# Performance work log

Hardware: AMD Instinct MI355X
Metric: run time of the kernel (lower is better)

## Reference

```python
import jax, jax.numpy as jnp
import numpy as np

AGENT_RADIUS = 0.2
SAFETY_DIST = 0.1
_ang = np.linspace(0.0, 2.0 * np.pi, 8, endpoint=False)
OBSTACLES = np.stack([10.0 * np.cos(_ang), 10.0 * np.sin(_ang), 0.5 * np.ones(8)], axis=-1).astype(np.float32)  # (x, y, r)


def _qp_solve(p, G, h):
    """Exact solve of: min_z 0.5 z^T z + p^T z  s.t. G z <= h, z in R^2.
    Equivalent to QPFunction with Q=I. Enumerates KKT candidates over active
    sets of size 0, 1, 2 (closed form in 2D) and picks the feasible optimum.
    p: [2], G: [m,2], h: [m]."""
    m = G.shape[0]
    ii, jj = np.triu_indices(m, 1)
    # active set {} -> unconstrained minimizer
    z0 = -p[None, :]                                        # [1,2]
    # active set {i}: z = -p - lam*g_i, g_i.z = h_i
    gg = jnp.sum(G * G, axis=-1)                            # [m]
    lam1 = (-(G @ p) - h) / (gg + 1e-12)
    z1 = -p[None, :] - lam1[:, None] * G                    # [m,2]
    ok1 = lam1 >= -1e-8
    # active set {i,j}: z solves 2x2 system [g_i; g_j] z = [h_i; h_j]
    Gi, Gj = G[ii], G[jj]                                   # [P,2]
    hi, hj = h[ii], h[jj]
    det = Gi[:, 0] * Gj[:, 1] - Gi[:, 1] * Gj[:, 0]
    det_ok = jnp.abs(det) > 1e-9
    ds = jnp.where(det_ok, det, 1.0)
    zx = (hi * Gj[:, 1] - hj * Gi[:, 1]) / ds
    zy = (Gi[:, 0] * hj - Gj[:, 0] * hi) / ds
    z2 = jnp.stack([zx, zy], axis=-1)                       # [P,2]
    r = -(z2 + p[None, :])                                  # A^T lam = r
    lam_i = (Gj[:, 1] * r[:, 0] - Gj[:, 0] * r[:, 1]) / ds
    lam_j = (Gi[:, 0] * r[:, 1] - Gi[:, 1] * r[:, 0]) / ds
    ok2 = det_ok & (lam_i >= -1e-8) & (lam_j >= -1e-8)
    Z = jnp.concatenate([z0, z1, z2], axis=0)               # [K,2]
    ok = jnp.concatenate([jnp.ones((1,), bool), ok1, ok2], axis=0)
    tol = 1e-6 * (1.0 + jnp.abs(h))
    feas = jnp.all(Z @ G.T <= (h + tol)[None, :], axis=-1)  # [K]
    obj = 0.5 * jnp.sum(Z * Z, axis=-1) + Z @ p
    obj = jnp.where(ok & feas, obj, jnp.inf)
    return Z[jnp.argmin(obj)]


def _forward(x, mean, std, W1, b1, W21, b21, W31, b31, W22, b22, W32, b32):
    x0 = x * std + mean                                     # de-normalized state [B,8]
    hid = jax.nn.relu(x @ W1.T + b1)
    x31 = jax.nn.relu(hid @ W21.T + b21) @ W31.T + b31      # reference control p [B,2]
    x32 = 4.0 * jax.nn.sigmoid(jax.nn.relu(hid @ W22.T + b22) @ W32.T + b32)  # CBF penalties [B,2]
    px, py, theta, v = x0[:, 0], x0[:, 1], x0[:, 2], x0[:, 3]
    ox, oy, oth, ov = x0[:, 4], x0[:, 5], x0[:, 6], x0[:, 7]
    st, ct = jnp.sin(theta), jnp.cos(theta)
    vs, vc = v * st, v * ct
    obs = jnp.asarray(OBSTACLES, x.dtype)
    # static obstacle constraints, vectorized over the n_obs obstacles
    dx = px[:, None] - obs[None, :, 0]                      # [B,n_obs]
    dy = py[:, None] - obs[None, :, 1]
    R = AGENT_RADIUS + obs[:, 2] + SAFETY_DIST
    bar = dx * dx + dy * dy - (R * R)[None, :]
    bdot = 2.0 * dx * vc[:, None] + 2.0 * dy * vs[:, None]
    Lf2b = (2.0 * v * v)[:, None]
    u1 = -2.0 * dx * vs[:, None] + 2.0 * dy * vc[:, None]
    u2 = 2.0 * dx * ct[:, None] + 2.0 * dy * st[:, None]
    G_obs = -jnp.stack([u1, u2], axis=-1)                   # [B,n_obs,2]
    s0, s1 = x32[:, 0:1], x32[:, 1:2]
    h_obs = Lf2b + (s0 + s1) * bdot + (s0 * s1) * bar       # [B,n_obs]
    # opponent constraint
    Ro = 2.0 * AGENT_RADIUS + SAFETY_DIST
    dxo, dyo = px - ox, py - oy
    so, co = jnp.sin(oth), jnp.cos(oth)
    bar_o = dxo * dxo + dyo * dyo - Ro * Ro
    bdot_o = 2.0 * dxo * (vc - ov * co) + 2.0 * dyo * (vs - ov * so)
    Lf2b_o = 2.0 * (v * v + ov * ov + 2.0 * v * ov * jnp.cos(theta - oth))
    u1o = -2.0 * dxo * vs + 2.0 * dyo * vc
    u2o = 2.0 * dxo * ct + 2.0 * dyo * st
    G_opp = -jnp.stack([u1o, u2o], axis=-1)[:, None, :]     # [B,1,2]
    h_opp = (Lf2b_o + (x32[:, 0] + x32[:, 1]) * bdot_o + x32[:, 0] * x32[:, 1] * bar_o)[:, None]
    G = jnp.concatenate([G_obs, G_opp], axis=1)             # [B,m,2]
    h = jnp.concatenate([h_obs, h_opp], axis=1)             # [B,m]
    return jax.vmap(_qp_solve)(x31, G, h)                   # [B,2]


def setup_inputs() -> dict:
    key = jax.random.key(0)
    ks = jax.random.split(key, 6)
    B, nF, H1, H2 = 65536, 8, 256, 128

    def lin(k, o, i):
        k1, k2 = jax.random.split(k)
        W = jax.random.normal(k1, (o, i), jnp.float32) / np.float32(np.sqrt(i))
        b = jax.random.normal(k2, (o,), jnp.float32) * 0.01
        return W, b

    W1, b1 = lin(ks[0], H1, nF)
    W21, b21 = lin(ks[1], H2, H1)
    W31, b31 = lin(ks[2], 2, H2)
    W22, b22 = lin(ks[3], H2, H1)
    W32, b32 = lin(ks[4], 2, H2)
    x = jax.random.normal(ks[5], (B, nF), jnp.float32)
    return {"x": x, "mean": jnp.zeros((nF,), jnp.float32), "std": jnp.ones((nF,), jnp.float32),
            "W1": W1, "b1": b1, "W21": W21, "b21": b21, "W31": W31, "b31": b31,
            "W22": W22, "b22": b22, "W32": W32, "b32": b32, "sgn": 1}


def reference(x, mean, std, W1, b1, W21, b21, W31, b31, W22, b22, W32, b32, sgn):
    # sgn==1 / training path -> batched differentiable QP solve
    return _forward(x, mean, std, W1, b1, W21, b21, W31, b31, W22, b22, W32, b32)
```

## Files before the change

### kernel.cpp

```cpp
#include <hip/hip_runtime.h>
#include <hip/hip_bf16.h>
#include <math.h>


typedef unsigned int u32;
typedef unsigned long long u64;
typedef unsigned short u16;
typedef __attribute__((ext_vector_type(8))) short short8;
typedef __attribute__((ext_vector_type(4))) float f32x4;
typedef __attribute__((ext_vector_type(2))) float f32x2;
typedef __attribute__((ext_vector_type(4))) u32 u32x4;

union Frag { short8 v; u32 u[4]; u32x4 q; };

__device__ __forceinline__ u32 packbf(float a, float b) {
    float2 f2; f2.x = a; f2.y = b;
    __hip_bfloat162 h = __float22bfloat162_rn(f2);
    union { __hip_bfloat162 h2; u32 u; } cv; cv.h2 = h;
    return cv.u;
}

__device__ const float OBX[8] = { 10.f, 7.07106781186547524f, 6.123234e-16f, -7.07106781186547524f,
                                 -10.f, -7.07106781186547524f, -1.8369702e-15f, 7.07106781186547524f };
__device__ const float OBY[8] = { 0.f, 7.07106781186547524f, 10.f, 7.07106781186547524f,
                                  1.2246468e-15f, -7.07106781186547524f, -10.f, -7.07106781186547524f };

#define PI0_ 0x2111111100000000ULL
#define PI1_ 0x5544443333322222ULL
#define PI2_ 0x7665ULL
#define PJ0_ 0x3876543287654321ULL
#define PJ1_ 0x7687658765487654ULL
#define PJ2_ 0x8878ULL
__device__ __forceinline__ int unpack4(u64 w0, u64 w1, u64 w2, int t) {
    u64 w = (t < 16) ? w0 : (t < 32) ? w1 : w2;
    return (int)((w >> ((t & 15) * 4)) & 15);
}

__global__ __launch_bounds__(256)
void prep_kernel(const float* __restrict__ W21, const float* __restrict__ W22,
                 u32* __restrict__ ws)
{
    int idx  = blockIdx.x * 256 + threadIdx.x;
    int lane = idx & 63;
    int nt   = (idx >> 6) & 7;
    int ks   = (idx >> 9) & 7;
    int head = idx >> 12;
    const float* W = head ? W22 : W21;
    int n  = nt * 16 + (lane & 15);
    int k0 = ks * 32 + (lane >> 4) * 8;
    const float* s = W + n * 256 + k0;
    u32x4 o;
    o.x = packbf(s[0], s[1]);
    o.y = packbf(s[2], s[3]);
    o.z = packbf(s[4], s[5]);
    o.w = packbf(s[6], s[7]);
    __builtin_nontemporal_store(o, (u32x4*)ws + idx);
}

__global__ __launch_bounds__(256)
void barriernet_kernel(const float* __restrict__ x,
                       const float* __restrict__ meanp,
                       const float* __restrict__ stdp,
                       const float* __restrict__ W1,
                       const float* __restrict__ b1,
                       const float* __restrict__ b21,
                       const float* __restrict__ W31,
                       const float* __restrict__ b31,
                       const float* __restrict__ b22,
                       const float* __restrict__ W32,
                       const float* __restrict__ b32,
                       const u32* __restrict__ wsB,
                       float* __restrict__ out, int Btot)
{
    const int tid  = threadIdx.x;
    const int wave = tid >> 6;
    const int lane = tid & 63;
    const int q    = lane >> 4;
    const int m    = lane & 15;
    const int blockRow = blockIdx.x * 64;

    __shared__ u32x4 stage[2048];
    __shared__ float lds_p[64][4];

    f32x4 xa0, xb0;
    {
        int R0 = blockRow + wave * 16 + m;
        const f32x4* xv0 = (const f32x4*)(x + (R0 < Btot ? R0 : 0) * 8);
        xa0 = xv0[0]; xb0 = xv0[1];
    }

    const f32x4* W1v = (const f32x4*)W1;
    const f32x4* b1v = (const f32x4*)b1;

    Frag A[8];
    #pragma unroll
    for (int ks = 0; ks < 8; ++ks) {
        int kb = ks * 32 + q * 8;
        f32x4 bA = b1v[kb >> 2];
        f32x4 bB = b1v[(kb >> 2) + 1];
        float h0[8];
        #pragma unroll
        for (int j = 0; j < 8; ++j) {
            f32x4 wa = W1v[(kb + j) * 2];
            f32x4 wb = W1v[(kb + j) * 2 + 1];
            float a0 = (j < 4) ? bA[j] : bB[j - 4];
            a0 = fmaf(wa.x, xa0.x, a0);
            a0 = fmaf(wa.y, xa0.y, a0);
            a0 = fmaf(wa.z, xa0.z, a0);
            a0 = fmaf(wa.w, xa0.w, a0);
            a0 = fmaf(wb.x, xb0.x, a0);
            a0 = fmaf(wb.y, xb0.y, a0);
            a0 = fmaf(wb.z, xb0.z, a0);
            a0 = fmaf(wb.w, xb0.w, a0);
            h0[j] = fmaxf(a0, 0.f);
        }
        #pragma unroll
        for (int t = 0; t < 4; ++t)
            A[ks].u[t] = packbf(h0[2 * t], h0[2 * t + 1]);
    }

    const u32x4* wsB4 = (const u32x4*)wsB;

    #pragma unroll 1
    for (int head = 0; head < 2; ++head) {
        const float* b2 = head ? b22 : b21;
        const float* W3 = head ? W32 : W31;
        const float* b3 = head ? b32 : b31;

        f32x4 acc[8];
        #pragma unroll
        for (int nt = 0; nt < 8; ++nt) acc[nt] = (f32x4){0.f, 0.f, 0.f, 0.f};

        #pragma unroll
        for (int half = 0; half < 2; ++half) {
            const u32x4* src = wsB4 + head * 4096 + half * 2048;
            #pragma unroll
            for (int i = 0; i < 8; ++i) {
                int fi = (wave * 8 + i) * 64 + lane;
                stage[fi] = src[fi];
            }
            __syncthreads();
            #pragma unroll
            for (int ksl = 0; ksl < 4; ++ksl) {
                const int ks = half * 4 + ksl;
                Frag Bf[8];
                #pragma unroll
                for (int nt = 0; nt < 8; ++nt)
                    Bf[nt].q = stage[ksl * 512 + nt * 64 + lane];
                #pragma unroll
                for (int nt = 0; nt < 8; ++nt)
                    acc[nt] = __builtin_amdgcn_mfma_f32_16x16x32_bf16(A[ks].v, Bf[nt].v, acc[nt], 0, 0, 0);
            }
            __syncthreads();
        }

        float pr0[4], pr1[4];
        #pragma unroll
        for (int rg = 0; rg < 4; ++rg) { pr0[rg] = 0.f; pr1[rg] = 0.f; }
        #pragma unroll
        for (int nt = 0; nt < 8; ++nt) {
            int col = nt * 16 + m;
            float b2c = b2[col];
            float w0c = W3[col];
            float w1c = W3[128 + col];
            #pragma unroll
            for (int rg = 0; rg < 4; ++rg) {
                float rv = fmaxf(acc[nt][rg] + b2c, 0.f);
                pr0[rg] = fmaf(rv, w0c, pr0[rg]);
                pr1[rg] = fmaf(rv, w1c, pr1[rg]);
            }
        }
        #pragma unroll
        for (int rg = 0; rg < 4; ++rg) {
            float v0 = pr0[rg], v1 = pr1[rg];
            #pragma unroll
            for (int off = 1; off < 16; off <<= 1) {
                v0 += __shfl_xor(v0, off, 64);
                v1 += __shfl_xor(v1, off, 64);
            }
            pr0[rg] = v0; pr1[rg] = v1;
        }
        if (m == 0) {
            #pragma unroll
            for (int rg = 0; rg < 4; ++rg) {
                int row = wave * 16 + q * 4 + rg;
                float a0 = pr0[rg] + b3[0];
                float a1 = pr1[rg] + b3[1];
                if (head == 0) {
                    lds_p[row][0] = a0;
                    lds_p[row][1] = a1;
                } else {
                    lds_p[row][2] = 4.f / (1.f + __expf(-a0));
                    lds_p[row][3] = 4.f / (1.f + __expf(-a1));
                }
            }
        }
    }
    __syncthreads();

    f32x4 (*qC)[64]  = (f32x4(*)[64])stage;
    f32x4 (*res)[64] = (f32x4(*)[64])(stage + 576);

    const int rq   = tid & 63;
    const int part = tid >> 6;
    const int R    = blockRow + rq;
    float p0 = lds_p[rq][0];
    float p1 = lds_p[rq][1];

    if (part == 0) {
        float s0 = lds_p[rq][2];
        float s1 = lds_p[rq][3];
        float xr[8];
        const float* xp = x + (R < Btot ? R : 0) * 8;
        #pragma unroll
        for (int c = 0; c < 8; ++c) xr[c] = fmaf(xp[c], stdp[c], meanp[c]);
        float px = xr[0], py = xr[1], th = xr[2], v = xr[3];
        float ox = xr[4], oy = xr[5], oth = xr[6], ov = xr[7];
        float st = __sinf(th),  ct = __cosf(th);
        float so = __sinf(oth), co = __cosf(oth);
        float vs = v * st, vc = v * ct;
        float sps = s0 + s1, ss = s0 * s1;
        float Lf2b = 2.f * v * v;
        #pragma unroll 1
        for (int k = 0; k < 8; ++k) {
            float dx = px - OBX[k], dy = py - OBY[k];
            float bar  = dx * dx + dy * dy - 0.64f;
            float bdot = 2.f * dx * vc + 2.f * dy * vs;
            float gx = 2.f * dx * vs - 2.f * dy * vc;
            float gy = -(2.f * dx * ct + 2.f * dy * st);
            float hk = Lf2b + sps * bdot + ss * bar;
            float ht = hk + 1e-6f * (1.f + fabsf(hk));
            qC[k][rq] = (f32x4){gx, gy, hk, ht};
        }
        {
            float dxo = px - ox, dyo = py - oy;
            float bar_o  = dxo * dxo + dyo * dyo - 0.25f;
            float bdot_o = 2.f * dxo * (vc - ov * co) + 2.f * dyo * (vs - ov * so);
            float Lf2b_o = 2.f * (v * v + ov * ov + 2.f * v * ov * __cosf(th - oth));
            float gx = 2.f * dxo * vs - 2.f * dyo * vc;
            float gy = -(2.f * dxo * ct + 2.f * dyo * st);
            float hk = Lf2b_o + sps * bdot_o + ss * bar_o;
            float ht = hk + 1e-6f * (1.f + fabsf(hk));
            qC[8][rq] = (f32x4){gx, gy, hk, ht};
        }
    }
    __syncthreads();

    const f32x4 C0 = qC[0][rq], C1 = qC[1][rq], C2 = qC[2][rq];
    const f32x4 C3 = qC[3][rq], C4 = qC[4][rq], C5 = qC[5][rq];
    const f32x4 C6 = qC[6][rq], C7 = qC[7][rq], C8 = qC[8][rq];

    const int c0i = (part == 0) ? 0  : (part == 1) ? 12 : (part == 2) ? 24 : 35;
    const int c1i = (part == 0) ? 12 : (part == 1) ? 24 : (part == 2) ? 35 : 46;
    float bobj = INFINITY;
    float bzx = -p0, bzy = -p1;
    #pragma unroll 2
    for (int c = c0i; c < c1i; ++c) {
        float zx, zy;
        bool pre;
        if (c == 0) {
            zx = -p0; zy = -p1; pre = true;
        } else if (c <= 9) {
            f32x4 g = qC[c - 1][rq];
            float gg  = g.x * g.x + g.y * g.y;
            float lam = (-(g.x * p0 + g.y * p1) - g.z) / (gg + 1e-12f);
            zx = -p0 - lam * g.x;
            zy = -p1 - lam * g.y;
            pre = (lam >= -1e-8f);
        } else {
            int t = c - 10;
            int pi = unpack4(PI0_, PI1_, PI2_, t);
            int pj = unpack4(PJ0_, PJ1_, PJ2_, t);
            f32x4 gi = qC[pi][rq];
            f32x4 gj = qC[pj][rq];
            float det = gi.x * gj.y - gi.y * gj.x;
            bool dok = fabsf(det) > 1e-9f;
            float ds = dok ? det : 1.0f;
            float inv = 1.0f / ds;
            zx = (gi.z * gj.y - gj.z * gi.y) * inv;
            zy = (gi.x * gj.z - gj.x * gi.z) * inv;
            float rx = -(zx + p0), ry = -(zy + p1);
            float li = (gj.y * rx - gj.x * ry) * inv;
            float lj = (gi.x * ry - gi.y * rx) * inv;
            pre = dok && (li >= -1e-8f) && (lj >= -1e-8f);
        }
        bool ok = pre;
        ok = ok && (zx * C0.x + zy * C0.y <= C0.w);
        ok = ok && (zx * C1.x + zy * C1.y <= C1.w);
        ok = ok && (zx * C2.x + zy * C2.y <= C2.w);
        ok = ok && (zx * C3.x + zy * C3.y <= C3.w);
        ok = ok && (zx * C4.x + zy * C4.y <= C4.w);
        ok = ok && (zx * C5.x + zy * C5.y <= C5.w);
        ok = ok && (zx * C6.x + zy * C6.y <= C6.w);
        ok = ok && (zx * C7.x + zy * C7.y <= C7.w);
        ok = ok && (zx * C8.x + zy * C8.y <= C8.w);
        float obj = 0.5f * (zx * zx + zy * zy) + zx * p0 + zy * p1;
        if (ok && obj < bobj) { bobj = obj; bzx = zx; bzy = zy; }
    }

    if (part) {
        res[part - 1][rq] = (f32x4){bobj, bzx, bzy, 0.f};
    }
    __syncthreads();
    if (part == 0) {
        #pragma unroll
        for (int pp = 0; pp < 3; ++pp) {
            f32x4 r = res[pp][rq];
            if (r.x < bobj) { bobj = r.x; bzx = r.y; bzy = r.z; }
        }
        if (R < Btot) {
            f32x2 o2; o2.x = bzx; o2.y = bzy;
            ((f32x2*)out)[R] = o2;
        }
    }
}

extern "C" void kernel_launch(void* const* d_in, const int* in_sizes, int n_in,
                              void* d_out, int out_size, void* d_ws, size_t ws_size,
                              hipStream_t stream) {
    const float* x    = (const float*)d_in[0];
    const float* mean = (const float*)d_in[1];
    const float* stdv = (const float*)d_in[2];
    const float* W1   = (const float*)d_in[3];
    const float* b1   = (const float*)d_in[4];
    const float* W21  = (const float*)d_in[5];
    const float* b21  = (const float*)d_in[6];
    const float* W31  = (const float*)d_in[7];
    const float* b31  = (const float*)d_in[8];
    const float* W22  = (const float*)d_in[9];
    const float* b22  = (const float*)d_in[10];
    const float* W32  = (const float*)d_in[11];
    const float* b32  = (const float*)d_in[12];
    int B = in_sizes[0] / 8;
    float* out = (float*)d_out;
    u32* ws = (u32*)d_ws;

    hipLaunchKernelGGL(prep_kernel, dim3(32), dim3(256), 0, stream, W21, W22, ws);

    hipLaunchKernelGGL(barriernet_kernel, dim3((B + 63) / 64), dim3(256), 0, stream,
                       x, mean, stdv, W1, b1, b21, W31, b31, b22, W32, b32,
                       ws, out, B);
}
```

Measured before the change: 117.5 us.

## Prefetch next weight chunk into registers and spread constraint setup across waves

Weight fragments for the next half-chunk are loaded into registers from global memory before the current chunk's MFMAs run, so the global load latency overlaps with compute instead of sitting between barriers. The first chunk is prefetched before the layer-1 computation. The obstacle-constraint setup, previously done by only one wave, is now split across all four waves, two obstacles each, with the opponent constraint on the last wave. This costs 8 extra vector registers of prefetch buffer, which could lower occupancy, and every wave now does redundant state loads and sin/cos work.

```diff
diff --git a/kernel.cpp b/kernel.cpp
--- a/kernel.cpp
+++ b/kernel.cpp
@@ -82,6 +82,13 @@
     __shared__ u32x4 stage[2048];
     __shared__ float lds_p[64][4];
 
+    const u32x4* wsB4 = (const u32x4*)wsB;
+
+    u32x4 pf[8];
+    #pragma unroll
+    for (int i = 0; i < 8; ++i)
+        pf[i] = wsB4[(wave * 8 + i) * 64 + lane];
+
     f32x4 xa0, xb0;
     {
         int R0 = blockRow + wave * 16 + m;
@@ -119,8 +126,6 @@
             A[ks].u[t] = packbf(h0[2 * t], h0[2 * t + 1]);
     }
 
-    const u32x4* wsB4 = (const u32x4*)wsB;
-
     #pragma unroll 1
     for (int head = 0; head < 2; ++head) {
         const float* b2 = head ? b22 : b21;
@@ -133,13 +138,20 @@
 
         #pragma unroll
         for (int half = 0; half < 2; ++half) {
-            const u32x4* src = wsB4 + head * 4096 + half * 2048;
-            #pragma unroll
-            for (int i = 0; i < 8; ++i) {
-                int fi = (wave * 8 + i) * 64 + lane;
-                stage[fi] = src[fi];
-            }
             __syncthreads();
+            #pragma unroll
+            for (int i = 0; i < 8; ++i)
+                stage[(wave * 8 + i) * 64 + lane] = pf[i];
+            __syncthreads();
+            {
+                const int p = head * 2 + half;
+                if (p < 3) {
+                    const u32x4* nsrc = wsB4 + (p + 1) * 2048 + lane;
+                    #pragma unroll
+                    for (int i = 0; i < 8; ++i)
+                        pf[i] = nsrc[(wave * 8 + i) * 64];
+                }
+            }
             #pragma unroll
             for (int ksl = 0; ksl < 4; ++ksl) {
                 const int ks = half * 4 + ksl;
@@ -151,7 +163,6 @@
                 for (int nt = 0; nt < 8; ++nt)
                     acc[nt] = __builtin_amdgcn_mfma_f32_16x16x32_bf16(A[ks].v, Bf[nt].v, acc[nt], 0, 0, 0);
             }
-            __syncthreads();
         }
 
         float pr0[4], pr1[4];
@@ -207,22 +218,29 @@
     float p0 = lds_p[rq][0];
     float p1 = lds_p[rq][1];
 
-    if (part == 0) {
+    {
         float s0 = lds_p[rq][2];
         float s1 = lds_p[rq][3];
-        float xr[8];
         const float* xp = x + (R < Btot ? R : 0) * 8;
-        #pragma unroll
-        for (int c = 0; c < 8; ++c) xr[c] = fmaf(xp[c], stdp[c], meanp[c]);
-        float px = xr[0], py = xr[1], th = xr[2], v = xr[3];
-        float ox = xr[4], oy = xr[5], oth = xr[6], ov = xr[7];
+        f32x4 xv0 = ((const f32x4*)xp)[0];
+        f32x4 xv1 = ((const f32x4*)xp)[1];
+        const f32x4 sd0 = ((const f32x4*)stdp)[0],  sd1 = ((const f32x4*)stdp)[1];
+        const f32x4 mn0 = ((const f32x4*)meanp)[0], mn1 = ((const f32x4*)meanp)[1];
+        float px = fmaf(xv0.x, sd0.x, mn0.x);
+        float py = fmaf(xv0.y, sd0.y, mn0.y);
+        float th = fmaf(xv0.z, sd0.z, mn0.z);
+        float v  = fmaf(xv0.w, sd0.w, mn0.w);
+        float ox = fmaf(xv1.x, sd1.x, mn1.x);
+        float oy = fmaf(xv1.y, sd1.y, mn1.y);
+        float oth= fmaf(xv1.z, sd1.z, mn1.z);
+        float ov = fmaf(xv1.w, sd1.w, mn1.w);
         float st = __sinf(th),  ct = __cosf(th);
-        float so = __sinf(oth), co = __cosf(oth);
         float vs = v * st, vc = v * ct;
         float sps = s0 + s1, ss = s0 * s1;
         float Lf2b = 2.f * v * v;
-        #pragma unroll 1
-        for (int k = 0; k < 8; ++k) {
+        #pragma unroll
+        for (int kk = 0; kk < 2; ++kk) {
+            int k = part + kk * 4;
             float dx = px - OBX[k], dy = py - OBY[k];
             float bar  = dx * dx + dy * dy - 0.64f;
             float bdot = 2.f * dx * vc + 2.f * dy * vs;
@@ -232,7 +250,8 @@
             float ht = hk + 1e-6f * (1.f + fabsf(hk));
             qC[k][rq] = (f32x4){gx, gy, hk, ht};
         }
-        {
+        if (part == 3) {
+            float so = __sinf(oth), co = __cosf(oth);
             float dxo = px - ox, dyo = py - oy;
             float bar_o  = dxo * dxo + dyo * dyo - 0.25f;
             float bdot_o = 2.f * dxo * (vc - ov * co) + 2.f * dyo * (vs - ov * so);
```

Result: slower. 124.8 us (+6.2%).

## Double block to 512 threads, splitting heads across waves and QP candidates eight ways

Applied to the files above, without the earlier changes.

Each block now runs 8 waves. Paired waves share a 16-row tile, and each wave of a pair computes only one of the two MLP heads, so the heads run concurrently instead of in a serial loop. Weight staging now streams both heads in four chunks, and the 46 QP candidates are split across 8 parts instead of 4, with a larger final reduction. The change raises parallelism per block and shortens per-wave serial work, at the cost of more barriers, more redundant first-layer compute (each row tile is computed by two waves), and possible LDS or register limits on occupancy.

```diff
diff --git a/kernel.cpp b/kernel.cpp
--- a/kernel.cpp
+++ b/kernel.cpp
@@ -57,7 +57,7 @@
     __builtin_nontemporal_store(o, (u32x4*)ws + idx);
 }
 
-__global__ __launch_bounds__(256)
+__global__ __launch_bounds__(512)
 void barriernet_kernel(const float* __restrict__ x,
                        const float* __restrict__ meanp,
                        const float* __restrict__ stdp,
@@ -77,6 +77,8 @@
     const int lane = tid & 63;
     const int q    = lane >> 4;
     const int m    = lane & 15;
+    const int rowtile = wave >> 1;
+    const int headw   = wave & 1;
     const int blockRow = blockIdx.x * 64;
 
     __shared__ u32x4 stage[2048];
@@ -84,7 +86,7 @@
 
     f32x4 xa0, xb0;
     {
-        int R0 = blockRow + wave * 16 + m;
+        int R0 = blockRow + rowtile * 16 + m;
         const f32x4* xv0 = (const f32x4*)(x + (R0 < Btot ? R0 : 0) * 8);
         xa0 = xv0[0]; xb0 = xv0[1];
     }
@@ -121,39 +123,42 @@
 
     const u32x4* wsB4 = (const u32x4*)wsB;
 
-    #pragma unroll 1
-    for (int head = 0; head < 2; ++head) {
-        const float* b2 = head ? b22 : b21;
-        const float* W3 = head ? W32 : W31;
-        const float* b3 = head ? b32 : b31;
-
-        f32x4 acc[8];
-        #pragma unroll
-        for (int nt = 0; nt < 8; ++nt) acc[nt] = (f32x4){0.f, 0.f, 0.f, 0.f};
-
-        #pragma unroll
-        for (int half = 0; half < 2; ++half) {
-            const u32x4* src = wsB4 + head * 4096 + half * 2048;
-            #pragma unroll
-            for (int i = 0; i < 8; ++i) {
-                int fi = (wave * 8 + i) * 64 + lane;
-                stage[fi] = src[fi];
+    const float* b2 = headw ? b22 : b21;
+    const float* W3 = headw ? W32 : W31;
+    const float* b3 = headw ? b32 : b31;
+
+    f32x4 acc[8];
+    #pragma unroll
+    for (int nt = 0; nt < 8; ++nt) acc[nt] = (f32x4){0.f, 0.f, 0.f, 0.f};
+
+    const int hb = headw * 1024;
+
+    #pragma unroll
+    for (int p = 0; p < 4; ++p) {
+        #pragma unroll
+        for (int h = 0; h < 2; ++h) {
+            #pragma unroll
+            for (int i = 0; i < 2; ++i) {
+                int j = i * 512 + tid;
+                stage[h * 1024 + j] = wsB4[h * 4096 + p * 1024 + j];
             }
-            __syncthreads();
-            #pragma unroll
-            for (int ksl = 0; ksl < 4; ++ksl) {
-                const int ks = half * 4 + ksl;
-                Frag Bf[8];
-                #pragma unroll
-                for (int nt = 0; nt < 8; ++nt)
-                    Bf[nt].q = stage[ksl * 512 + nt * 64 + lane];
-                #pragma unroll
-                for (int nt = 0; nt < 8; ++nt)
-                    acc[nt] = __builtin_amdgcn_mfma_f32_16x16x32_bf16(A[ks].v, Bf[nt].v, acc[nt], 0, 0, 0);
-            }
-            __syncthreads();
-        }
-
+        }
+        __syncthreads();
+        #pragma unroll
+        for (int ksl = 0; ksl < 2; ++ksl) {
+            const int ks = p * 2 + ksl;
+            Frag Bf[8];
+            #pragma unroll
+            for (int nt = 0; nt < 8; ++nt)
+                Bf[nt].q = stage[hb + ksl * 512 + nt * 64 + lane];
+            #pragma unroll
+            for (int nt = 0; nt < 8; ++nt)
+                acc[nt] = __builtin_amdgcn_mfma_f32_16x16x32_bf16(A[ks].v, Bf[nt].v, acc[nt], 0, 0, 0);
+        }
+        __syncthreads();
+    }
+
+    {
         float pr0[4], pr1[4];
         #pragma unroll
         for (int rg = 0; rg < 4; ++rg) { pr0[rg] = 0.f; pr1[rg] = 0.f; }
@@ -183,10 +188,10 @@
         if (m == 0) {
             #pragma unroll
             for (int rg = 0; rg < 4; ++rg) {
-                int row = wave * 16 + q * 4 + rg;
+                int row = rowtile * 16 + q * 4 + rg;
                 float a0 = pr0[rg] + b3[0];
                 float a1 = pr1[rg] + b3[1];
-                if (head == 0) {
+                if (headw == 0) {
                     lds_p[row][0] = a0;
                     lds_p[row][1] = a1;
                 } else {
@@ -250,8 +255,10 @@
     const f32x4 C3 = qC[3][rq], C4 = qC[4][rq], C5 = qC[5][rq];
     const f32x4 C6 = qC[6][rq], C7 = qC[7][rq], C8 = qC[8][rq];
 
-    const int c0i = (part == 0) ? 0  : (part == 1) ? 12 : (part == 2) ? 24 : 35;
-    const int c1i = (part == 0) ? 12 : (part == 1) ? 24 : (part == 2) ? 35 : 46;
+    const u64 BNDS = (7ULL << 6) | (13ULL << 12) | (19ULL << 18) | (25ULL << 24)
+                   | (31ULL << 30) | (36ULL << 36) | (41ULL << 42) | (46ULL << 48);
+    const int c0i = (int)((BNDS >> (6 * part)) & 63);
+    const int c1i = (int)((BNDS >> (6 * part + 6)) & 63);
     float bobj = INFINITY;
     float bzx = -p0, bzy = -p1;
     #pragma unroll 2
@@ -304,7 +311,7 @@
     __syncthreads();
     if (part == 0) {
         #pragma unroll
-        for (int pp = 0; pp < 3; ++pp) {
+        for (int pp = 0; pp < 7; ++pp) {
             f32x4 r = res[pp][rq];
             if (r.x < bobj) { bobj = r.x; bzx = r.y; bzy = r.z; }
         }
@@ -337,7 +344,7 @@
 
     hipLaunchKernelGGL(prep_kernel, dim3(32), dim3(256), 0, stream, W21, W22, ws);
 
-    hipLaunchKernelGGL(barriernet_kernel, dim3((B + 63) / 64), dim3(256), 0, stream,
+    hipLaunchKernelGGL(barriernet_kernel, dim3((B + 63) / 64), dim3(512), 0, stream,
                        x, mean, stdv, W1, b1, b21, W31, b31, b22, W32, b32,
                        ws, out, B);
 }
```

Result: slower. 141.0 us (+20.0%).
